# Kernel optimization log

Measured on AMD Instinct MI355X. Metric: run time of the kernel, lower is better.

## Reference

```python
import jax, jax.numpy as jnp
import numpy as np

# Config derived from init_kwargs (see get_window_sizes):
GROUP = 1
HEADS = 2
NUM_BSWIN = 4
C = 8                     # channels per (bswin, head)
BIG = [3, 6, 12, 24]      # big window sizes (cubic)
SMALL = [1, 2, 4, 8]      # small window (max-pool kernel) sizes
NWIN = 3                  # big/small per dim -> 3x3x3 tokens per window
L = GROUP * NWIN ** 3     # 27 tokens per attention window


def setup_inputs() -> dict:
    key = jax.random.key(0)
    k1, k2, k3, k4 = jax.random.split(key, 4)
    shape = (4, 64, 48, 48, 48)
    return {
        "query": jax.random.normal(k1, shape, dtype=jnp.float32),
        "key": jax.random.normal(k2, shape, dtype=jnp.float32),
        "value": jax.random.normal(k3, shape, dtype=jnp.float32),
        # Swin-style relative position bias table: (2*3-1)^3 = 125 entries, per head
        "rpb_table": jax.random.normal(k4, (125, HEADS), dtype=jnp.float32) * 0.02,
    }


def _rel_bias(table):
    # relative position index for a 3x3x3 window -> (HEADS, 27, 27)
    r = jnp.arange(NWIN)
    coords = jnp.stack(jnp.meshgrid(r, r, r, indexing="ij")).reshape(3, -1)  # (3,27)
    rel = coords[:, :, None] - coords[:, None, :] + (NWIN - 1)  # in [0, 4]
    idx = (rel[0] * (2 * NWIN - 1) + rel[1]) * (2 * NWIN - 1) + rel[2]
    return table[idx].transpose(2, 0, 1)  # (HEADS, 27, 27)


def _gather(x):
    # x: (b, in_ch, h, w, d) -> (b, HEADS, sum_N, L, C), Ns
    b, _, h, w, d = x.shape
    x = x.reshape(b, GROUP, NUM_BSWIN, HEADS, C, h, w, d)
    xs, Ns = [], []
    for i in range(NUM_BSWIN):
        bw, sw = BIG[i], SMALL[i]
        Nh, Nw, Nd = h // bw, w // bw, d // bw
        xi = x[:, :, i]  # (b,G,H,C,h,w,d)
        # split into big windows and max-pool small windows (kernel=stride=sw)
        xi = xi.reshape(b, GROUP, HEADS, C, Nh, NWIN, sw, Nw, NWIN, sw, Nd, NWIN, sw)
        xi = xi.max(axis=(6, 9, 12))  # (b,G,H,C,Nh,3,Nw,3,Nd,3)
        # -> (b, H, Nh, Nw, Nd, G, nh, nw, nd, C)
        xi = xi.transpose(0, 2, 4, 6, 8, 1, 5, 7, 9, 3)
        xs.append(xi.reshape(b, HEADS, Nh * Nw * Nd, L, C))
        Ns.append((Nh, Nw, Nd))
    return jnp.concatenate(xs, axis=2), Ns


def _upsample_axis(x, axis, out_size):
    # 1D linear interpolation, align_corners=True
    in_size = x.shape[axis]
    if out_size == in_size:
        return x
    pos = jnp.linspace(0.0, in_size - 1.0, out_size)
    i0 = jnp.floor(pos).astype(jnp.int32)
    i1 = jnp.minimum(i0 + 1, in_size - 1)
    wgt = (pos - i0).astype(x.dtype)
    shape = [1] * x.ndim
    shape[axis] = out_size
    wgt = wgt.reshape(shape)
    return jnp.take(x, i0, axis=axis) * (1 - wgt) + jnp.take(x, i1, axis=axis) * wgt


def _scatter(outs, Ns):
    # outs: (b, HEADS, sum_N, L, C) -> (b, in_ch, h, w, d)
    b = outs.shape[0]
    outs = outs.reshape(b, HEADS, -1, GROUP, NWIN, NWIN, NWIN, C)
    idx, parts = 0, []
    for i in range(NUM_BSWIN):
        Nh, Nw, Nd = Ns[i]
        N = Nh * Nw * Nd
        sw = SMALL[i]
        o = outs[:, :, idx:idx + N]  # (b,H,N,G,3,3,3,C)
        o = o.transpose(0, 3, 1, 2, 7, 4, 5, 6)  # (b,G,H,N,C,3,3,3)
        for ax in (5, 6, 7):  # trilinear upsample, align_corners=True
            o = _upsample_axis(o, ax, NWIN * sw)
        o = o.reshape(b, GROUP, HEADS, Nh, Nw, Nd, C, NWIN * sw, NWIN * sw, NWIN * sw)
        # -> (b,G,H,C, Nh,winh, Nw,winw, Nd,wind)
        o = o.transpose(0, 1, 2, 6, 3, 7, 4, 8, 5, 9)
        parts.append(o.reshape(b, GROUP, HEADS, C, Nh * NWIN * sw, Nw * NWIN * sw, Nd * NWIN * sw))
        idx += N
    out = jnp.stack(parts, axis=2)  # (b, G, bswin, H, C, h, w, d)
    return out.reshape(b, GROUP * NUM_BSWIN * HEADS * C, *out.shape[-3:])


def _forward(query, key, value, rpb_table):
    q, Ns = _gather(query)
    k, _ = _gather(key)
    v, _ = _gather(value)
    scale = jnp.sqrt(jnp.asarray(C, q.dtype))
    scores = jnp.einsum("bhNmc,bhNnc->bhNmn", q, k)
    weights = jax.nn.softmax(scores / scale, axis=-1)
    # NOTE: bias is added AFTER softmax in the original module (faithful)
    weights = weights + _rel_bias(rpb_table)[None, :, None]  # (1,H,1,27,27)
    attn = jnp.einsum("bhNmn,bhNnc->bhNmc", weights, v)
    return _scatter(attn, Ns)


def reference(query, key, value, rpb_table):
    return _forward(query, key, value, rpb_table)
```

## Files before the change

kernel.cpp:

```cpp
#include <hip/hip_runtime.h>
#include <math.h>


#define NTOT 4680
#define NWINDOWS_TOTAL 37440
#define GATHER_ELEMS 8087040

__global__ void pool0_kernel(const float* __restrict__ q,
                             const float* __restrict__ k,
                             const float* __restrict__ v,
                             float* __restrict__ qg,
                             float* __restrict__ kg,
                             float* __restrict__ vg)
{
    __shared__ float lds[9216];

    unsigned int bid = blockIdx.x;
    int yh = bid & 1;  bid >>= 1;
    int z  = bid % 48; bid /= 48;
    int hd = bid & 1;  bid >>= 1;
    int b  = bid & 3;  bid >>= 2;
    int t  = (int)bid;

    const float* src = (t == 0) ? q : (t == 1) ? k : v;
    float*       dst = (t == 0) ? qg : (t == 1) ? kg : vg;

    int tid = threadIdx.x;
    const float* gsrc = src + ((size_t)(b * 64 + hd * 8) * 48 + z) * 2304 + yh * 1152;

    #pragma unroll
    for (int j = 0; j < 9; j++) {
        int f  = tid + 256 * j;
        int c  = f / 288;
        int r  = f - c * 288;
        int y  = r / 12;
        int xq = r - y * 12;
        float4 val = *(const float4*)(gsrc + (size_t)c * 110592 + y * 48 + xq * 4);
        int key   = xq & 7;
        int gbase = (y * 48 + xq * 4) * 2 + (c >> 2);
        int csub  = c & 3;
        lds[((gbase + 0) ^ key) * 4 + csub] = val.x;
        lds[((gbase + 2) ^ key) * 4 + csub] = val.y;
        lds[((gbase + 4) ^ key) * 4 + csub] = val.z;
        lds[((gbase + 6) ^ key) * 4 + csub] = val.w;
    }
    __syncthreads();

    int nh = z / 3, lh = z - nh * 3;
    int bh = b * 2 + hd;
    float4* dst4 = (float4*)dst;
    #pragma unroll
    for (int j = 0; j < 9; j++) {
        int cw     = tid + 256 * j;
        int window = cw / 18;
        int off    = cw - window * 18;
        int chalf  = off & 1;
        int t2     = off >> 1;
        int ld     = t2 % 3;
        int lw     = t2 / 3;
        int nw_loc = window >> 4;
        int nd     = window & 15;
        int yl = nw_loc * 3 + lw;
        int x  = nd * 3 + ld;
        int g  = (yl * 48 + x) * 2 + chalf;
        int gs = g ^ ((x >> 2) & 7);
        float4 val = *(const float4*)&lds[gs * 4];
        int n = nh * 256 + (yh * 8 + nw_loc) * 16 + nd;
        dst4[((size_t)bh * NTOT + n) * 54 + lh * 18 + off] = val;
    }
}

template<int SW, int NC, int NOFF, int SCALE>
__device__ __forceinline__ void pool_impl(const float* __restrict__ q,
                                          const float* __restrict__ k,
                                          const float* __restrict__ v,
                                          float* __restrict__ qg,
                                          float* __restrict__ kg,
                                          float* __restrict__ vg,
                                          unsigned int tid)
{
    const int BW = SW * 3;
    int c  = tid % 8;  tid /= 8;
    int ld = tid % 3;  tid /= 3;
    int nd = tid % NC; tid /= NC;
    int lw = tid % 3;  tid /= 3;
    int nw = tid % NC; tid /= NC;
    int lh = tid % 3;  tid /= 3;
    int nh = tid % NC; tid /= NC;
    int hd = tid % 2;  tid /= 2;
    int b  = tid % 2;  tid /= 2;
    b += (int)(tid % 2) * 2;
    int t  = (int)(tid / 2);

    const float* src = (t == 0) ? q : (t == 1) ? k : v;
    float*       dst = (t == 0) ? qg : (t == 1) ? kg : vg;

    int ch = SCALE * 16 + hd * 8 + c;
    int z0 = nh * BW + lh * SW;
    int y0 = nw * BW + lw * SW;
    int x0 = nd * BW + ld * SW;

    const float* base = src + ((((b * 64 + ch) * 48 + z0) * 48 + y0) * 48 + x0);

    float m = -INFINITY;
    if constexpr (SW == 2) {
        #pragma unroll
        for (int dz = 0; dz < 2; dz++) {
            #pragma unroll
            for (int dy = 0; dy < 2; dy++) {
                float2 p = *(const float2*)(base + (dz * 48 + dy) * 48);
                m = fmaxf(m, fmaxf(p.x, p.y));
            }
        }
    } else {
        #pragma unroll
        for (int dz = 0; dz < SW; dz++) {
            #pragma unroll
            for (int dy = 0; dy < SW; dy++) {
                #pragma unroll
                for (int dx = 0; dx < SW; dx += 4) {
                    float4 p = *(const float4*)(base + (dz * 48 + dy) * 48 + dx);
                    m = fmaxf(m, fmaxf(fmaxf(p.x, p.y), fmaxf(p.z, p.w)));
                }
            }
        }
    }

    int n = (nh * NC + nw) * NC + nd + NOFF;
    int l = (lh * 3 + lw) * 3 + ld;
    dst[(((b * 2 + hd) * NTOT + n) * 27 + l) * 8 + c] = m;
}

#define RB1 10368u
#define RB2 11664u
#define RB3 11826u

__global__ void pool_rest(const float* __restrict__ q,
                          const float* __restrict__ k,
                          const float* __restrict__ v,
                          float* __restrict__ qg,
                          float* __restrict__ kg,
                          float* __restrict__ vg)
{
    unsigned int bid = blockIdx.x;
    if (bid < RB1) {
        pool_impl<2, 8, 4096, 1>(q, k, v, qg, kg, vg, bid * 256 + threadIdx.x);
    } else if (bid < RB2) {
        pool_impl<4, 4, 4608, 2>(q, k, v, qg, kg, vg, (bid - RB1) * 256 + threadIdx.x);
    } else {
        pool_impl<8, 2, 4672, 3>(q, k, v, qg, kg, vg, (bid - RB2) * 256 + threadIdx.x);
    }
}

__global__ void attn_kernel(float* qg,
                            const float* __restrict__ kg,
                            const float* __restrict__ vg,
                            const float* __restrict__ rpb)
{
    __shared__ float4 ks[432];
    __shared__ float4 vs[432];
    __shared__ float4 qs[432];
    __shared__ float tbl[250];

    int tid = threadIdx.x;
    int wbase = blockIdx.x * 8;
    int hd = (blockIdx.x / 585) & 1;

    for (int i = tid; i < 250; i += 256) tbl[i] = rpb[i];
    {
        const float4* kg4 = (const float4*)kg + (size_t)wbase * 54;
        const float4* vg4 = (const float4*)vg + (size_t)wbase * 54;
        const float4* qg4 = (const float4*)qg + (size_t)wbase * 54;
        for (int i = tid; i < 432; i += 256) {
            ks[i] = kg4[i];
            vs[i] = vg4[i];
            qs[i] = qg4[i];
        }
    }
    __syncthreads();

    int widx = tid >> 5;
    int m    = tid & 31;
    if (m < 27) {
        float4 q0 = qs[widx * 54 + m * 2];
        float4 q1 = qs[widx * 54 + m * 2 + 1];

        const float inv_scale = 0.35355339059327373f;
        float s[27];
        float mx = -INFINITY;
        #pragma unroll
        for (int n = 0; n < 27; n++) {
            float4 k0 = ks[widx * 54 + n * 2];
            float4 k1 = ks[widx * 54 + n * 2 + 1];
            float acc = q0.x * k0.x + q0.y * k0.y + q0.z * k0.z + q0.w * k0.w
                      + q1.x * k1.x + q1.y * k1.y + q1.z * k1.z + q1.w * k1.w;
            acc *= inv_scale;
            s[n] = acc;
            mx = fmaxf(mx, acc);
        }
        float sum = 0.f;
        #pragma unroll
        for (int n = 0; n < 27; n++) { s[n] = __expf(s[n] - mx); sum += s[n]; }
        float inv = 1.f / sum;

        int mz = m / 9, my = (m / 3) % 3, mxx = m % 3;
        int mbase = ((mz + 2) * 5 + (my + 2)) * 5 + (mxx + 2);

        float4 a0 = make_float4(0.f, 0.f, 0.f, 0.f);
        float4 a1 = make_float4(0.f, 0.f, 0.f, 0.f);
        #pragma unroll
        for (int n = 0; n < 27; n++) {
            const int nz = n / 9, ny = (n / 3) % 3, nx = n % 3;
            const int nconst = (nz * 5 + ny) * 5 + nx;
            float wgt = s[n] * inv + tbl[(mbase - nconst) * 2 + hd];
            float4 v0 = vs[widx * 54 + n * 2];
            float4 v1 = vs[widx * 54 + n * 2 + 1];
            a0.x += wgt * v0.x; a0.y += wgt * v0.y; a0.z += wgt * v0.z; a0.w += wgt * v0.w;
            a1.x += wgt * v1.x; a1.y += wgt * v1.y; a1.z += wgt * v1.z; a1.w += wgt * v1.w;
        }
        qs[widx * 54 + m * 2]     = a0;
        qs[widx * 54 + m * 2 + 1] = a1;
    }
    __syncthreads();

    float4* og4 = (float4*)qg + (size_t)wbase * 54;
    for (int i = tid; i < 432; i += 256) og4[i] = qs[i];
}

template<int SCALE>
__device__ __forceinline__ void scatter_impl(const float* __restrict__ attn,
                                             float* __restrict__ out,
                                             unsigned int tid)
{
    constexpr int BW   = (SCALE == 0) ? 3 : (SCALE == 1) ? 6 : (SCALE == 2) ? 12 : 24;
    constexpr int NC   = 16 >> SCALE;
    constexpr int NOFF = (SCALE == 0) ? 0 : (SCALE == 1) ? 4096 : (SCALE == 2) ? 4608 : 4672;
    const float ST = 2.0f / (float)(BW - 1);

    int xq  = tid % 12; tid /= 12;
    int y   = tid % 48; tid /= 48;
    int z   = tid % 48; tid /= 48;
    int chi = tid % 16; tid /= 16;
    int b   = (int)tid;

    int hd = chi >> 3, c = chi & 7;

    int nh = z / BW, pz = z - nh * BW;
    int nw = y / BW, py = y - nw * BW;

    int z0 = 0, z1 = 0, y0 = 0, y1 = 0;
    float wz = 0.f, wy = 0.f;
    if constexpr (SCALE != 0) {
        float fz = pz * ST; z0 = (int)fz; if (z0 > 2) z0 = 2; wz = fz - z0; z1 = min(z0 + 1, 2);
        float fy = py * ST; y0 = (int)fy; if (y0 > 2) y0 = 2; wy = fy - y0; y1 = min(y0 + 1, 2);
    }

    float res[4];
    #pragma unroll
    for (int j = 0; j < 4; j++) {
        int x  = xq * 4 + j;
        int nd = x / BW, px = x - nd * BW;
        int n  = (nh * NC + nw) * NC + nd + NOFF;
        const float* a = attn + (((size_t)(b * 2 + hd) * NTOT + n) * 216) + c;
        if constexpr (SCALE == 0) {
            res[j] = a[((pz * 3 + py) * 3 + px) * 8];
        } else {
            float fx = px * ST; int x0 = (int)fx; if (x0 > 2) x0 = 2;
            float wx = fx - x0; int x1 = min(x0 + 1, 2);
            #define AT(iz, iy, ix) a[(((iz) * 3 + (iy)) * 3 + (ix)) * 8]
            float c00 = AT(z0, y0, x0) * (1.f - wx) + AT(z0, y0, x1) * wx;
            float c01 = AT(z0, y1, x0) * (1.f - wx) + AT(z0, y1, x1) * wx;
            float c10 = AT(z1, y0, x0) * (1.f - wx) + AT(z1, y0, x1) * wx;
            float c11 = AT(z1, y1, x0) * (1.f - wx) + AT(z1, y1, x1) * wx;
            float c0  = c00 * (1.f - wy) + c01 * wy;
            float c1  = c10 * (1.f - wy) + c11 * wy;
            res[j] = c0 * (1.f - wz) + c1 * wz;
            #undef AT
        }
    }

    size_t ob = ((((size_t)(b * 64 + SCALE * 16 + chi) * 48 + z) * 48 + y) * 48) + xq * 4;
    *(float4*)(out + ob) = make_float4(res[0], res[1], res[2], res[3]);
}

#define SBLK 6912u

__global__ void scatter_all(const float* __restrict__ attn,
                            float* __restrict__ out)
{
    unsigned int bid = blockIdx.x;
    if (bid < SBLK) {
        scatter_impl<0>(attn, out, bid * 256 + threadIdx.x);
    } else if (bid < 2 * SBLK) {
        scatter_impl<1>(attn, out, (bid - SBLK) * 256 + threadIdx.x);
    } else if (bid < 3 * SBLK) {
        scatter_impl<2>(attn, out, (bid - 2 * SBLK) * 256 + threadIdx.x);
    } else {
        scatter_impl<3>(attn, out, (bid - 3 * SBLK) * 256 + threadIdx.x);
    }
}

extern "C" void kernel_launch(void* const* d_in, const int* in_sizes, int n_in,
                              void* d_out, int out_size, void* d_ws, size_t ws_size,
                              hipStream_t stream)
{
    const float* q   = (const float*)d_in[0];
    const float* k   = (const float*)d_in[1];
    const float* v   = (const float*)d_in[2];
    const float* rpb = (const float*)d_in[3];
    float* out = (float*)d_out;

    float* qg = (float*)d_ws;
    float* kg = qg + GATHER_ELEMS;
    float* vg = kg + GATHER_ELEMS;

    pool0_kernel<<<2304, 256, 0, stream>>>(q, k, v, qg, kg, vg);
    pool_rest<<<RB3, 256, 0, stream>>>(q, k, v, qg, kg, vg);
    attn_kernel<<<NWINDOWS_TOTAL / 8, 256, 0, stream>>>(qg, kg, vg, rpb);
    scatter_all<<<4 * SBLK, 256, 0, stream>>>(qg, out);
}
```

Measured before the change: 570.1 us.

## Fuse pool, attention and scatter for small-window scales into one LDS kernel

Scales 0 and 1, which hold most of the windows, now run in a single kernel. Each block loads a row of windows straight from the inputs into shared memory (max-pooling on load for scale 1), computes the attention there, and writes the upsampled output directly. This removes the workspace round-trip for gathered q/k/v and attention output at those scales. Scales 2 and 3 keep the separate pool/attn/scatter path, with pool thread indexing reordered so nd varies fastest. The cost is larger blocks with about 42KB of LDS each, lower occupancy, and less coalesced global loads in the fused kernel.

```diff
diff --git a/kernel.cpp b/kernel.cpp
--- a/kernel.cpp
+++ b/kernel.cpp
@@ -3,94 +3,210 @@
 
 
 #define NTOT 4680
-#define NWINDOWS_TOTAL 37440
 #define GATHER_ELEMS 8087040
 
-__global__ void pool0_kernel(const float* __restrict__ q,
-                             const float* __restrict__ k,
-                             const float* __restrict__ v,
-                             float* __restrict__ qg,
-                             float* __restrict__ kg,
-                             float* __restrict__ vg)
-{
-    __shared__ float lds[9216];
-
+template<int SW>
+__device__ __forceinline__ void fused_body(const float* __restrict__ q,
+                                           const float* __restrict__ k,
+                                           const float* __restrict__ v,
+                                           const float* __restrict__ rpb,
+                                           float* __restrict__ out,
+                                           unsigned int bid,
+                                           float* qs, float* ks, float* vs,
+                                           float* tbl)
+{
+    constexpr int SCALE = (SW == 1) ? 0 : 1;
+    constexpr int NC    = (SW == 1) ? 16 : 8;
+    constexpr int NWIN  = NC;
+    int tid = threadIdx.x;
+
+    int nw = bid % NC; bid /= NC;
+    int nh = bid % NC; bid /= NC;
+    int bh = (int)bid;
+    int b = bh >> 1, hd = bh & 1;
+    int chb = SCALE * 16 + hd * 8;
+
+    for (int i = tid; i < 250; i += 512) tbl[i] = rpb[i];
+
+    if constexpr (SW == 1) {
+        for (int i = tid; i < 2592; i += 512) {
+            int t = i / 864;
+            int r = i - t * 864;
+            int c = r / 108; r -= c * 108;
+            int z = r / 36;  r -= z * 36;
+            int y = r / 12;
+            int xq = r - y * 12;
+            const float* src = (t == 0) ? q : (t == 1) ? k : v;
+            float* dst = (t == 0) ? qs : (t == 1) ? ks : vs;
+            const float* p = src + (((size_t)(b * 64 + chb + c) * 48 + nh * 3 + z) * 48
+                                    + nw * 3 + y) * 48 + xq * 4;
+            float4 val = *(const float4*)p;
+            float tmp[4] = {val.x, val.y, val.z, val.w};
+            #pragma unroll
+            for (int e = 0; e < 4; e++) {
+                int x = xq * 4 + e;
+                int w = x / 3, ld = x - w * 3;
+                dst[(w * 27 + z * 9 + y * 3 + ld) * 8 + c] = tmp[e];
+            }
+        }
+    } else {
+        for (int i = tid; i < 5184; i += 512) {
+            int t = i / 1728;
+            int r = i - t * 1728;
+            int c  = r / 216; r -= c * 216;
+            int lz = r / 72;  r -= lz * 72;
+            int ly = r / 24;
+            int xc = r - ly * 24;
+            const float* src = (t == 0) ? q : (t == 1) ? k : v;
+            float* dst = (t == 0) ? qs : (t == 1) ? ks : vs;
+            const float* base = src + (((size_t)(b * 64 + chb + c) * 48 + nh * 6 + lz * 2) * 48
+                                       + nw * 6 + ly * 2) * 48 + xc * 2;
+            float m = -INFINITY;
+            #pragma unroll
+            for (int dz = 0; dz < 2; dz++) {
+                #pragma unroll
+                for (int dy = 0; dy < 2; dy++) {
+                    float2 p2 = *(const float2*)(base + (dz * 48 + dy) * 48);
+                    m = fmaxf(m, fmaxf(p2.x, p2.y));
+                }
+            }
+            int w = xc / 3, ld = xc - w * 3;
+            dst[(w * 27 + lz * 9 + ly * 3 + ld) * 8 + c] = m;
+        }
+    }
+    __syncthreads();
+
+    {
+        int widx = tid >> 5, m = tid & 31;
+        if (widx < NWIN && m < 27) {
+            float4 q0 = *(float4*)&qs[(widx * 27 + m) * 8];
+            float4 q1 = *(float4*)&qs[(widx * 27 + m) * 8 + 4];
+            const float inv_scale = 0.35355339059327373f;
+            float s[27], mx = -INFINITY;
+            #pragma unroll
+            for (int n = 0; n < 27; n++) {
+                float4 k0 = *(float4*)&ks[(widx * 27 + n) * 8];
+                float4 k1 = *(float4*)&ks[(widx * 27 + n) * 8 + 4];
+                float acc = q0.x * k0.x + q0.y * k0.y + q0.z * k0.z + q0.w * k0.w
+                          + q1.x * k1.x + q1.y * k1.y + q1.z * k1.z + q1.w * k1.w;
+                acc *= inv_scale;
+                s[n] = acc; mx = fmaxf(mx, acc);
+            }
+            float sum = 0.f;
+            #pragma unroll
+            for (int n = 0; n < 27; n++) { s[n] = __expf(s[n] - mx); sum += s[n]; }
+            float inv = 1.f / sum;
+
+            int mz = m / 9, my = (m / 3) % 3, mxx = m % 3;
+            int mbase = ((mz + 2) * 5 + (my + 2)) * 5 + (mxx + 2);
+
+            float4 a0 = make_float4(0.f, 0.f, 0.f, 0.f);
+            float4 a1 = make_float4(0.f, 0.f, 0.f, 0.f);
+            #pragma unroll
+            for (int n = 0; n < 27; n++) {
+                const int nz = n / 9, ny = (n / 3) % 3, nx = n % 3;
+                const int nconst = (nz * 5 + ny) * 5 + nx;
+                float wgt = s[n] * inv + tbl[(mbase - nconst) * 2 + hd];
+                float4 v0 = *(float4*)&vs[(widx * 27 + n) * 8];
+                float4 v1 = *(float4*)&vs[(widx * 27 + n) * 8 + 4];
+                a0.x += wgt * v0.x; a0.y += wgt * v0.y; a0.z += wgt * v0.z; a0.w += wgt * v0.w;
+                a1.x += wgt * v1.x; a1.y += wgt * v1.y; a1.z += wgt * v1.z; a1.w += wgt * v1.w;
+            }
+            *(float4*)&qs[(widx * 27 + m) * 8]     = a0;
+            *(float4*)&qs[(widx * 27 + m) * 8 + 4] = a1;
+        }
+    }
+    __syncthreads();
+
+    if constexpr (SW == 1) {
+        for (int i = tid; i < 864; i += 512) {
+            int c = i / 108;
+            int r = i - c * 108;
+            int zz = r / 36; r -= zz * 36;
+            int yy = r / 12;
+            int xq = r - yy * 12;
+            float res[4];
+            #pragma unroll
+            for (int e = 0; e < 4; e++) {
+                int x = xq * 4 + e;
+                int w = x / 3, ld = x - w * 3;
+                res[e] = qs[(w * 27 + zz * 9 + yy * 3 + ld) * 8 + c];
+            }
+            float* po = out + (((size_t)(b * 64 + chb + c) * 48 + nh * 3 + zz) * 48
+                               + nw * 3 + yy) * 48 + xq * 4;
+            *(float4*)po = make_float4(res[0], res[1], res[2], res[3]);
+        }
+    } else {
+        const float ST = 2.0f / 5.0f;
+        for (int i = tid; i < 3456; i += 512) {
+            int c = i / 432;
+            int r = i - c * 432;
+            int zz = r / 72; r -= zz * 72;
+            int yy = r / 12;
+            int xq = r - yy * 12;
+            float fz = zz * ST; int z0 = (int)fz; if (z0 > 2) z0 = 2;
+            float wz = fz - z0; int z1 = min(z0 + 1, 2);
+            float fy = yy * ST; int y0 = (int)fy; if (y0 > 2) y0 = 2;
+            float wy = fy - y0; int y1 = min(y0 + 1, 2);
+            float res[4];
+            #pragma unroll
+            for (int e = 0; e < 4; e++) {
+                int x = xq * 4 + e;
+                int w = x / 6, px = x - w * 6;
+                float fx = px * ST; int x0 = (int)fx; if (x0 > 2) x0 = 2;
+                float wx = fx - x0; int x1 = min(x0 + 1, 2);
+                const float* a = &qs[w * 216 + c];
+                #define AT(iz, iy, ix) a[(((iz) * 3 + (iy)) * 3 + (ix)) * 8]
+                float c00 = AT(z0, y0, x0) * (1.f - wx) + AT(z0, y0, x1) * wx;
+                float c01 = AT(z0, y1, x0) * (1.f - wx) + AT(z0, y1, x1) * wx;
+                float c10 = AT(z1, y0, x0) * (1.f - wx) + AT(z1, y0, x1) * wx;
+                float c11 = AT(z1, y1, x0) * (1.f - wx) + AT(z1, y1, x1) * wx;
+                float c0  = c00 * (1.f - wy) + c01 * wy;
+                float c1  = c10 * (1.f - wy) + c11 * wy;
+                res[e] = c0 * (1.f - wz) + c1 * wz;
+                #undef AT
+            }
+            float* po = out + (((size_t)(b * 64 + chb + c) * 48 + nh * 6 + zz) * 48
+                               + nw * 6 + yy) * 48 + xq * 4;
+            *(float4*)po = make_float4(res[0], res[1], res[2], res[3]);
+        }
+    }
+}
+
+__global__ __launch_bounds__(512)
+void fused01_kernel(const float* __restrict__ q, const float* __restrict__ k,
+                    const float* __restrict__ v, const float* __restrict__ rpb,
+                    float* __restrict__ out)
+{
+    __shared__ __align__(16) float qs[3456];
+    __shared__ __align__(16) float ks[3456];
+    __shared__ __align__(16) float vs[3456];
+    __shared__ float tbl[250];
     unsigned int bid = blockIdx.x;
-    int yh = bid & 1;  bid >>= 1;
-    int z  = bid % 48; bid /= 48;
-    int hd = bid & 1;  bid >>= 1;
-    int b  = bid & 3;  bid >>= 2;
-    int t  = (int)bid;
-
-    const float* src = (t == 0) ? q : (t == 1) ? k : v;
-    float*       dst = (t == 0) ? qg : (t == 1) ? kg : vg;
-
-    int tid = threadIdx.x;
-    const float* gsrc = src + ((size_t)(b * 64 + hd * 8) * 48 + z) * 2304 + yh * 1152;
-
-    #pragma unroll
-    for (int j = 0; j < 9; j++) {
-        int f  = tid + 256 * j;
-        int c  = f / 288;
-        int r  = f - c * 288;
-        int y  = r / 12;
-        int xq = r - y * 12;
-        float4 val = *(const float4*)(gsrc + (size_t)c * 110592 + y * 48 + xq * 4);
-        int key   = xq & 7;
-        int gbase = (y * 48 + xq * 4) * 2 + (c >> 2);
-        int csub  = c & 3;
-        lds[((gbase + 0) ^ key) * 4 + csub] = val.x;
-        lds[((gbase + 2) ^ key) * 4 + csub] = val.y;
-        lds[((gbase + 4) ^ key) * 4 + csub] = val.z;
-        lds[((gbase + 6) ^ key) * 4 + csub] = val.w;
-    }
-    __syncthreads();
-
-    int nh = z / 3, lh = z - nh * 3;
-    int bh = b * 2 + hd;
-    float4* dst4 = (float4*)dst;
-    #pragma unroll
-    for (int j = 0; j < 9; j++) {
-        int cw     = tid + 256 * j;
-        int window = cw / 18;
-        int off    = cw - window * 18;
-        int chalf  = off & 1;
-        int t2     = off >> 1;
-        int ld     = t2 % 3;
-        int lw     = t2 / 3;
-        int nw_loc = window >> 4;
-        int nd     = window & 15;
-        int yl = nw_loc * 3 + lw;
-        int x  = nd * 3 + ld;
-        int g  = (yl * 48 + x) * 2 + chalf;
-        int gs = g ^ ((x >> 2) & 7);
-        float4 val = *(const float4*)&lds[gs * 4];
-        int n = nh * 256 + (yh * 8 + nw_loc) * 16 + nd;
-        dst4[((size_t)bh * NTOT + n) * 54 + lh * 18 + off] = val;
-    }
+    if (bid < 2048) fused_body<1>(q, k, v, rpb, out, bid, qs, ks, vs, tbl);
+    else            fused_body<2>(q, k, v, rpb, out, bid - 2048, qs, ks, vs, tbl);
 }
 
 template<int SW, int NC, int NOFF, int SCALE>
-__device__ __forceinline__ void pool_impl(const float* __restrict__ q,
-                                          const float* __restrict__ k,
-                                          const float* __restrict__ v,
-                                          float* __restrict__ qg,
-                                          float* __restrict__ kg,
-                                          float* __restrict__ vg,
-                                          unsigned int tid)
+__device__ __forceinline__ void pool23_impl(const float* __restrict__ q,
+                                            const float* __restrict__ k,
+                                            const float* __restrict__ v,
+                                            float* __restrict__ qg,
+                                            float* __restrict__ kg,
+                                            float* __restrict__ vg,
+                                            unsigned int tid)
 {
     const int BW = SW * 3;
-    int c  = tid % 8;  tid /= 8;
     int ld = tid % 3;  tid /= 3;
     int nd = tid % NC; tid /= NC;
+    int c  = tid % 8;  tid /= 8;
     int lw = tid % 3;  tid /= 3;
     int nw = tid % NC; tid /= NC;
     int lh = tid % 3;  tid /= 3;
     int nh = tid % NC; tid /= NC;
     int hd = tid % 2;  tid /= 2;
-    int b  = tid % 2;  tid /= 2;
-    b += (int)(tid % 2) * 2;
-    int t  = (int)(tid / 2);
+    int b  = tid % 4;  tid /= 4;
+    int t  = (int)tid;
 
     const float* src = (t == 0) ? q : (t == 1) ? k : v;
     float*       dst = (t == 0) ? qg : (t == 1) ? kg : vg;
@@ -100,62 +216,45 @@
     int y0 = nw * BW + lw * SW;
     int x0 = nd * BW + ld * SW;
 
-    const float* base = src + ((((b * 64 + ch) * 48 + z0) * 48 + y0) * 48 + x0);
+    const float* base = src + ((((size_t)(b * 64 + ch) * 48 + z0) * 48 + y0) * 48 + x0);
 
     float m = -INFINITY;
-    if constexpr (SW == 2) {
+    #pragma unroll
+    for (int dz = 0; dz < SW; dz++) {
         #pragma unroll
-        for (int dz = 0; dz < 2; dz++) {
-            #pragma unroll
-            for (int dy = 0; dy < 2; dy++) {
-                float2 p = *(const float2*)(base + (dz * 48 + dy) * 48);
-                m = fmaxf(m, fmaxf(p.x, p.y));
-            }
-        }
-    } else {
-        #pragma unroll
-        for (int dz = 0; dz < SW; dz++) {
-            #pragma unroll
-            for (int dy = 0; dy < SW; dy++) {
-                #pragma unroll
-                for (int dx = 0; dx < SW; dx += 4) {
-                    float4 p = *(const float4*)(base + (dz * 48 + dy) * 48 + dx);
-                    m = fmaxf(m, fmaxf(fmaxf(p.x, p.y), fmaxf(p.z, p.w)));
-                }
+        for (int dy = 0; dy < SW; dy++) {
+            #pragma unroll
+            for (int dx = 0; dx < SW; dx += 4) {
+                float4 p = *(const float4*)(base + (dz * 48 + dy) * 48 + dx);
+                m = fmaxf(m, fmaxf(fmaxf(p.x, p.y), fmaxf(p.z, p.w)));
             }
         }
     }
 
     int n = (nh * NC + nw) * NC + nd + NOFF;
     int l = (lh * 3 + lw) * 3 + ld;
-    dst[(((b * 2 + hd) * NTOT + n) * 27 + l) * 8 + c] = m;
-}
-
-#define RB1 10368u
-#define RB2 11664u
-#define RB3 11826u
-
-__global__ void pool_rest(const float* __restrict__ q,
-                          const float* __restrict__ k,
-                          const float* __restrict__ v,
-                          float* __restrict__ qg,
-                          float* __restrict__ kg,
-                          float* __restrict__ vg)
+    dst[((((size_t)(b * 2 + hd)) * NTOT + n) * 27 + l) * 8 + c] = m;
+}
+
+#define P23_B2 1296u
+#define P23_B3 1458u
+
+__global__ void pool23_kernel(const float* __restrict__ q,
+                              const float* __restrict__ k,
+                              const float* __restrict__ v,
+                              float* __restrict__ qg,
+                              float* __restrict__ kg,
+                              float* __restrict__ vg)
 {
     unsigned int bid = blockIdx.x;
-    if (bid < RB1) {
-        pool_impl<2, 8, 4096, 1>(q, k, v, qg, kg, vg, bid * 256 + threadIdx.x);
-    } else if (bid < RB2) {
-        pool_impl<4, 4, 4608, 2>(q, k, v, qg, kg, vg, (bid - RB1) * 256 + threadIdx.x);
-    } else {
-        pool_impl<8, 2, 4672, 3>(q, k, v, qg, kg, vg, (bid - RB2) * 256 + threadIdx.x);
-    }
-}
-
-__global__ void attn_kernel(float* qg,
-                            const float* __restrict__ kg,
-                            const float* __restrict__ vg,
-                            const float* __restrict__ rpb)
+    if (bid < P23_B2) pool23_impl<4, 4, 4608, 2>(q, k, v, qg, kg, vg, bid * 256 + threadIdx.x);
+    else              pool23_impl<8, 2, 4672, 3>(q, k, v, qg, kg, vg, (bid - P23_B2) * 256 + threadIdx.x);
+}
+
+__global__ void attn23_kernel(float* qg,
+                              const float* __restrict__ kg,
+                              const float* __restrict__ vg,
+                              const float* __restrict__ rpb)
 {
     __shared__ float4 ks[432];
     __shared__ float4 vs[432];
@@ -163,8 +262,10 @@
     __shared__ float tbl[250];
 
     int tid = threadIdx.x;
-    int wbase = blockIdx.x * 8;
-    int hd = (blockIdx.x / 585) & 1;
+    int j  = blockIdx.x;
+    int bh = j / 9;
+    int wbase = bh * NTOT + 4608 + (j - bh * 9) * 8;
+    int hd = bh & 1;
 
     for (int i = tid; i < 250; i += 256) tbl[i] = rpb[i];
     {
@@ -186,8 +287,7 @@
         float4 q1 = qs[widx * 54 + m * 2 + 1];
 
         const float inv_scale = 0.35355339059327373f;
-        float s[27];
-        float mx = -INFINITY;
+        float s[27], mx = -INFINITY;
         #pragma unroll
         for (int n = 0; n < 27; n++) {
             float4 k0 = ks[widx * 54 + n * 2];
@@ -195,8 +295,7 @@
             float acc = q0.x * k0.x + q0.y * k0.y + q0.z * k0.z + q0.w * k0.w
                       + q1.x * k1.x + q1.y * k1.y + q1.z * k1.z + q1.w * k1.w;
             acc *= inv_scale;
-            s[n] = acc;
-            mx = fmaxf(mx, acc);
+            s[n] = acc; mx = fmaxf(mx, acc);
         }
         float sum = 0.f;
         #pragma unroll
@@ -232,9 +331,9 @@
                                              float* __restrict__ out,
                                              unsigned int tid)
 {
-    constexpr int BW   = (SCALE == 0) ? 3 : (SCALE == 1) ? 6 : (SCALE == 2) ? 12 : 24;
+    constexpr int BW   = (SCALE == 2) ? 12 : 24;
     constexpr int NC   = 16 >> SCALE;
-    constexpr int NOFF = (SCALE == 0) ? 0 : (SCALE == 1) ? 4096 : (SCALE == 2) ? 4608 : 4672;
+    constexpr int NOFF = (SCALE == 2) ? 4608 : 4672;
     const float ST = 2.0f / (float)(BW - 1);
 
     int xq  = tid % 12; tid /= 12;
@@ -248,12 +347,10 @@
     int nh = z / BW, pz = z - nh * BW;
     int nw = y / BW, py = y - nw * BW;
 
-    int z0 = 0, z1 = 0, y0 = 0, y1 = 0;
-    float wz = 0.f, wy = 0.f;
-    if constexpr (SCALE != 0) {
-        float fz = pz * ST; z0 = (int)fz; if (z0 > 2) z0 = 2; wz = fz - z0; z1 = min(z0 + 1, 2);
-        float fy = py * ST; y0 = (int)fy; if (y0 > 2) y0 = 2; wy = fy - y0; y1 = min(y0 + 1, 2);
-    }
+    float fz = pz * ST; int z0 = (int)fz; if (z0 > 2) z0 = 2;
+    float wz = fz - z0; int z1 = min(z0 + 1, 2);
+    float fy = py * ST; int y0 = (int)fy; if (y0 > 2) y0 = 2;
+    float wy = fy - y0; int y1 = min(y0 + 1, 2);
 
     float res[4];
     #pragma unroll
@@ -262,21 +359,17 @@
         int nd = x / BW, px = x - nd * BW;
         int n  = (nh * NC + nw) * NC + nd + NOFF;
         const float* a = attn + (((size_t)(b * 2 + hd) * NTOT + n) * 216) + c;
-        if constexpr (SCALE == 0) {
-            res[j] = a[((pz * 3 + py) * 3 + px) * 8];
-        } else {
-            float fx = px * ST; int x0 = (int)fx; if (x0 > 2) x0 = 2;
-            float wx = fx - x0; int x1 = min(x0 + 1, 2);
-            #define AT(iz, iy, ix) a[(((iz) * 3 + (iy)) * 3 + (ix)) * 8]
-            float c00 = AT(z0, y0, x0) * (1.f - wx) + AT(z0, y0, x1) * wx;
-            float c01 = AT(z0, y1, x0) * (1.f - wx) + AT(z0, y1, x1) * wx;
-            float c10 = AT(z1, y0, x0) * (1.f - wx) + AT(z1, y0, x1) * wx;
-            float c11 = AT(z1, y1, x0) * (1.f - wx) + AT(z1, y1, x1) * wx;
-            float c0  = c00 * (1.f - wy) + c01 * wy;
-            float c1  = c10 * (1.f - wy) + c11 * wy;
-            res[j] = c0 * (1.f - wz) + c1 * wz;
-            #undef AT
-        }
+        float fx = px * ST; int x0 = (int)fx; if (x0 > 2) x0 = 2;
+        float wx = fx - x0; int x1 = min(x0 + 1, 2);
+        #define AT(iz, iy, ix) a[(((iz) * 3 + (iy)) * 3 + (ix)) * 8]
+        float c00 = AT(z0, y0, x0) * (1.f - wx) + AT(z0, y0, x1) * wx;
+        float c01 = AT(z0, y1, x0) * (1.f - wx) + AT(z0, y1, x1) * wx;
+        float c10 = AT(z1, y0, x0) * (1.f - wx) + AT(z1, y0, x1) * wx;
+        float c11 = AT(z1, y1, x0) * (1.f - wx) + AT(z1, y1, x1) * wx;
+        float c0  = c00 * (1.f - wy) + c01 * wy;
+        float c1  = c10 * (1.f - wy) + c11 * wy;
+        res[j] = c0 * (1.f - wz) + c1 * wz;
+        #undef AT
     }
 
     size_t ob = ((((size_t)(b * 64 + SCALE * 16 + chi) * 48 + z) * 48 + y) * 48) + xq * 4;
@@ -285,19 +378,12 @@
 
 #define SBLK 6912u
 
-__global__ void scatter_all(const float* __restrict__ attn,
-                            float* __restrict__ out)
+__global__ void scatter23_kernel(const float* __restrict__ attn,
+                                 float* __restrict__ out)
 {
     unsigned int bid = blockIdx.x;
-    if (bid < SBLK) {
-        scatter_impl<0>(attn, out, bid * 256 + threadIdx.x);
-    } else if (bid < 2 * SBLK) {
-        scatter_impl<1>(attn, out, (bid - SBLK) * 256 + threadIdx.x);
-    } else if (bid < 3 * SBLK) {
-        scatter_impl<2>(attn, out, (bid - 2 * SBLK) * 256 + threadIdx.x);
-    } else {
-        scatter_impl<3>(attn, out, (bid - 3 * SBLK) * 256 + threadIdx.x);
-    }
+    if (bid < SBLK) scatter_impl<2>(attn, out, bid * 256 + threadIdx.x);
+    else            scatter_impl<3>(attn, out, (bid - SBLK) * 256 + threadIdx.x);
 }
 
 extern "C" void kernel_launch(void* const* d_in, const int* in_sizes, int n_in,
@@ -314,8 +400,9 @@
     float* kg = qg + GATHER_ELEMS;
     float* vg = kg + GATHER_ELEMS;
 
-    pool0_kernel<<<2304, 256, 0, stream>>>(q, k, v, qg, kg, vg);
-    pool_rest<<<RB3, 256, 0, stream>>>(q, k, v, qg, kg, vg);
-    attn_kernel<<<NWINDOWS_TOTAL / 8, 256, 0, stream>>>(qg, kg, vg, rpb);
-    scatter_all<<<4 * SBLK, 256, 0, stream>>>(qg, out);
-}
+    fused01_kernel<<<2560, 512, 0, stream>>>(q, k, v, rpb, out);
+
+    pool23_kernel<<<P23_B3, 256, 0, stream>>>(q, k, v, qg, kg, vg);
+    attn23_kernel<<<72, 256, 0, stream>>>(qg, kg, vg, rpb);
+    scatter23_kernel<<<2 * SBLK, 256, 0, stream>>>(qg, out);
+}
```

Result: faster. 465.4 us (-18.4%).
